# Optimization experiments

Measured on AMD Instinct MI355X. Metric: run time of the kernel, lower is better.

## Reference

```python
import math
import jax, jax.numpy as jnp
import numpy as np

B, N, D = 16, 2048, 256
EPS = 1e-8  # torch cosine_similarity default eps
TAU = 3.0   # gumbel-softmax temperature


def setup_inputs() -> dict:
    key = jax.random.key(0)
    k1, k2 = jax.random.split(key)
    return {
        "LowLevelFeatures": jax.random.normal(k1, (B, 1, N, D), dtype=jnp.float32),
        "HighLevelFeatures": jax.random.normal(k2, (B, 1, N, D), dtype=jnp.float32),
        "batch_size": B,
    }


def _forward(LLF4, HLF4):
    LLF = LLF4[:, 0]  # [B,N,D]
    HLF = HLF4[:, 0]  # [B,N,D]
    b, n, d = LLF.shape
    # pairwise cosine similarity [B,N,N]: matmul + norm-product (same math as
    # torch's broadcast cosine_similarity, without the [B,N,N,D] intermediate)
    dots = jnp.einsum('bnd,bmd->bnm', LLF, HLF)
    nl = jnp.linalg.norm(LLF, axis=-1)  # [B,N]
    nh = jnp.linalg.norm(HLF, axis=-1)  # [B,N]
    sim = dots / jnp.maximum(nl[:, :, None] * nh[:, None, :], EPS)
    sim = sim / math.sqrt(d)
    probs = jax.nn.softmax(sim, axis=1)  # softmax over dim 1 (LLF rows)
    # F.gumbel_softmax(probs, tau=3, hard=True, dim=1): probs act as logits
    u = jax.random.uniform(jax.random.key(42), probs.shape,
                           minval=1e-10, maxval=1.0)
    gumbels = -jnp.log(-jnp.log(u))
    y_soft = jax.nn.softmax((probs + gumbels) / TAU, axis=1)
    idx = jnp.argmax(y_soft, axis=1)  # [B,N]: selected LLF-row n per HLF col m
    # torch.where on the one-hot scans row-major over (b, n, m), so per batch
    # the returned n-indices are the SORTED multiset of selected indices
    sl = jnp.sort(idx, axis=-1)  # [B,N]
    bidx = jnp.arange(b)[:, None]  # [B,1]
    aligned = HLF[bidx, sl]  # gather along dim 1 -> [B,N,D]
    # rowwise cosine similarity between gathered HLF and LLF
    w = jnp.sum(aligned * LLF, axis=-1) / jnp.maximum(
        jnp.linalg.norm(aligned, axis=-1) * nl, EPS)  # [B,N]
    noise = jax.nn.softmax(w / 0.1, axis=1)[:, :, None]  # [B,N,1]
    hlf_new = aligned + LLF * noise
    out = HLF.at[bidx, sl].set(hlf_new)
    return out


def reference(LowLevelFeatures, HighLevelFeatures, batch_size):
    return _forward(LowLevelFeatures, HighLevelFeatures)
```

## Files before the change

### kernel.cpp

```cpp
#include <hip/hip_runtime.h>
#include <math.h>

#define NB 16
#define NN 2048
#define ND 256
#define BNtot (NB*NN)
#define HH 33554432u

__device__ __forceinline__ unsigned rotl(unsigned v, int r){
  return __builtin_amdgcn_alignbit(v, v, 32-r);
}
__device__ __forceinline__ unsigned umaxu(unsigned a, unsigned b){ return a > b ? a : b; }
__device__ __forceinline__ unsigned uminu(unsigned a, unsigned b){ return a < b ? a : b; }

__device__ __forceinline__ float gumbelv(unsigned b, unsigned n, unsigned m){
  unsigned f = (b<<22) | (n<<11) | m;
  unsigned x0 = (b < 8u) ? f : (f - HH);
  unsigned x1 = x0 + HH;
  const unsigned ks0=0u, ks1=42u, ks2=0u^42u^0x1BD11BDAu;
  unsigned v0 = x0 + ks0;
  unsigned v1 = x1 + ks1;
#define TFR(r) { v0 += v1; v1 = rotl(v1,(r)); v1 ^= v0; }
  TFR(13) TFR(15) TFR(26) TFR(6)
  v0 += ks1; v1 += ks2 + 1u;
  TFR(17) TFR(29) TFR(16) TFR(24)
  v0 += ks2; v1 += ks0 + 2u;
  TFR(13) TFR(15) TFR(26) TFR(6)
  v0 += ks0; v1 += ks1 + 3u;
  TFR(17) TFR(29) TFR(16) TFR(24)
  v0 += ks1; v1 += ks2 + 4u;
  TFR(13) TFR(15) TFR(26) TFR(6)
  v0 += ks2; v1 += ks0 + 5u;
#undef TFR
  unsigned bits = (b < 8u) ? v0 : v1;
  float fl = __uint_as_float((bits>>9) | 0x3F800000u) - 1.0f;
  float u = fmaxf(1e-10f, fl + 1e-10f);
  return -logf(-logf(u));
}

__device__ __forceinline__ float gfromkey(unsigned key){
  float fl = __uint_as_float(key | 0x3F800000u) - 1.0f;
  float u = fmaxf(1e-10f, fl + 1e-10f);
  return -logf(-logf(u));
}

struct GumState {
  unsigned x0, vk, a1, a2, c1, c2;
  int t;
};

__device__ __forceinline__ void gum_init(GumState& g, int t){
  g.t = t;
  int half = t & 1;
  int m    = (t >> 1) & 2047;
  int bl   = (t >> 12) & 7;
  int nq   = t >> 15;
  int nstart = (nq << 7) + (half << 6);
  g.x0 = ((unsigned)bl << 22) | ((unsigned)nstart << 11) | (unsigned)m;
  g.a1 = g.a2 = g.c1 = g.c2 = 0;
  g.vk = (unsigned)(127 - (half<<6));
}

__device__ __forceinline__ void gum_iter(GumState& g, const int cnt){
  const unsigned KS2 = 42u ^ 0x1BD11BDAu;
  unsigned x0=g.x0, vk=g.vk, a1=g.a1, a2=g.a2, c1=g.c1, c2=g.c2;
#define TFR(r)       { v0 += v1; v1 = rotl(v1,(r)); v1 ^= v0; }
#define TFRI(r, inj) { v0 += v1 + (inj); v1 = rotl(v1,(r)); v1 ^= v0; }
  #pragma unroll 4
  for (int j = 0; j < cnt; ++j){
    unsigned v0 = x0;
    unsigned v1 = x0 + (HH + 42u);
    TFR(13) TFR(15) TFR(26) TFR(6)
    v1 += KS2 + 1u;
    TFRI(17, 42u) TFR(29) TFR(16) TFR(24)
    v1 += 2u;
    TFRI(13, KS2) TFR(15) TFR(26) TFR(6)
    v1 += 42u + 3u;
    TFR(17) TFR(29) TFR(16) TFR(24)
    v1 += KS2 + 4u;
    TFRI(13, 42u) TFR(15) TFR(26) TFR(6)
    v0 += KS2; v1 += 5u;
    unsigned pa = (v0 & 0xFFFFFE00u) | vk;
    unsigned pb = (v1 & 0xFFFFFE00u) | vk;
    unsigned ta = uminu(pa, a1);
    a1 = umaxu(pa, a1);
    a2 = umaxu(ta, a2);
    unsigned tc = uminu(pb, c1);
    c1 = umaxu(pb, c1);
    c2 = umaxu(tc, c2);
    x0 += 2048u;
    vk -= 1u;
  }
#undef TFR
#undef TFRI
  g.x0=x0; g.vk=vk; g.a1=a1; g.a2=a2; g.c1=c1; g.c2=c2;
}

__device__ __forceinline__ void gum_finish(const GumState& g, unsigned* __restrict__ pck){
  int half = g.t & 1;
  int m    = (g.t >> 1) & 2047;
  int bl   = (g.t >> 12) & 7;
  int nq   = g.t >> 15;
  unsigned p1 = __shfl_xor((int)g.a1, 1), p2 = __shfl_xor((int)g.a2, 1);
  unsigned q1 = __shfl_xor((int)g.c1, 1), q2 = __shfl_xor((int)g.c2, 1);
  unsigned A1 = umaxu(g.a1, p1);
  unsigned A2 = umaxu(uminu(g.a1, p1), umaxu(g.a2, p2));
  unsigned C1 = umaxu(g.c1, q1);
  unsigned C2 = umaxu(uminu(g.c1, q1), umaxu(g.c2, q2));
  if (half == 0){
    uint2 ua; ua.x = A1; ua.y = A2;
    uint2 uc; uc.x = C1; uc.y = C2;
    *(uint2*)(&pck[((size_t)bl*NN + m)*32 + (nq<<1)])     = ua;
    *(uint2*)(&pck[((size_t)(bl+8)*NN + m)*32 + (nq<<1)]) = uc;
  }
}

__device__ __forceinline__ void norm_rows(const float4* v, int wid, int lane,
                                          float* __restrict__ nrm){
  #pragma unroll
  for (int i=0;i<4;i++){
    float s = v[i].x*v[i].x + v[i].y*v[i].y + v[i].z*v[i].z + v[i].w*v[i].w;
    for (int o=32;o;o>>=1) s += __shfl_down(s,o);
    if (lane==0) nrm[wid*4 + i] = sqrtf(s);
  }
}

__global__ void knorms(const float* __restrict__ LLF, const float* __restrict__ HLF,
                       float* __restrict__ nl, float* __restrict__ nh){
  int row = blockIdx.x;
  int wave = threadIdx.x >> 6;
  int lane = threadIdx.x & 63;
  const float* src = wave ? HLF : LLF;
  float4 v = ((const float4*)(src + (size_t)row*ND))[lane];
  float s = v.x*v.x + v.y*v.y + v.z*v.z + v.w*v.w;
  for (int o=32;o;o>>=1) s += __shfl_down(s,o);
  if (lane==0) (wave? nh: nl)[row] = sqrtf(s);
}

__launch_bounds__(256, 8)
__global__ void kfuse1(const float* __restrict__ LLF, const float* __restrict__ HLF,
                       float* __restrict__ nl, float* __restrict__ nh,
                       unsigned* __restrict__ pck){
  int t = blockIdx.x*256 + (int)threadIdx.x;
  int wid = t >> 6;
  int lane = t & 63;
  GumState g; gum_init(g, t);
  float4 va[4];
  #pragma unroll
  for (int i=0;i<4;i++)
    va[i] = ((const float4*)(LLF + (size_t)(wid*4+i)*ND))[lane];
  gum_iter(g, 32);
  norm_rows(va, wid, lane, nl);
  float4 vb[4];
  #pragma unroll
  for (int i=0;i<4;i++)
    vb[i] = ((const float4*)(HLF + (size_t)(wid*4+i)*ND))[lane];
  gum_iter(g, 32);
  norm_rows(vb, wid, lane, nh);
  gum_finish(g, pck);
}

#define ILO 4.882e-4f
#define IHI 5.534e-4f
__launch_bounds__(256)
__global__ void kresolve(const float* __restrict__ LLF, const float* __restrict__ HLF,
                         const float* __restrict__ nl, const float* __restrict__ nh,
                         const unsigned* __restrict__ pck,
                         int* __restrict__ idx){
  __shared__ float hsAll[4][ND];
  int w    = threadIdx.x >> 6;
  int lane = threadIdx.x & 63;
  int g = blockIdx.x*4 + w;
  int b = g >> 11;
  float pv = -INFINITY; int pn = 0;
  if (lane < 32){
    unsigned pk = pck[(size_t)g*32 + lane];
    pv = gfromkey(pk >> 9);
    pn = ((lane >> 1) << 7) + 127 - (int)(pk & 127u);
  }
  float gmax = pv;
  for (int o=32;o;o>>=1) gmax = fmaxf(gmax, __shfl_down(gmax,o));
  gmax = __shfl(gmax, 0);
  unsigned long long mask = __ballot(pv >= gmax - 8e-5f) & 0xFFFFFFFFull;
  if (__popcll(mask) == 1){
    int src = __builtin_ctzll(mask);
    int n = __shfl(pn, src);
    if (lane==0) idx[g] = n;
    return;
  }
  float4 h = ((const float4*)(HLF + (size_t)g*ND))[lane];
  float nhg = nh[g];
  float bestLo = -INFINITY, bestHi = -INFINITY;
  int nLo = 1<<30, nHi = 1<<30;
  unsigned long long mm = mask;
  while (mm){
    int src = __builtin_ctzll(mm); mm &= mm-1;
    int   n  = __shfl(pn, src);
    float gv = __shfl(pv, src);
    float4 a = ((const float4*)(LLF + ((size_t)b*NN + n)*ND))[lane];
    float d = a.x*h.x + a.y*h.y + a.z*h.z + a.w*h.w;
    for (int o=32;o;o>>=1) d += __shfl_down(d,o);
    d = __shfl(d, 0);
    float sim = (d / fmaxf(nl[b*NN+n]*nhg, 1e-8f)) * 0.0625f;
    float e = expf(sim - 0.0625f);
    float qlo = e*ILO + gv;
    float qhi = e*IHI + gv;
    if (qlo > bestLo || (qlo == bestLo && n < nLo)){ bestLo = qlo; nLo = n; }
    if (qhi > bestHi || (qhi == bestHi && n < nHi)){ bestHi = qhi; nHi = n; }
  }
  if (nLo == nHi){
    if (lane==0) idx[g] = nLo;
    return;
  }
  float* hs = hsAll[w];
  *(float4*)(&hs[lane<<2]) = h;
  float S = 0.0f;
  for (int r = 0; r < 32; ++r){
    int n2 = (r<<6) + lane;
    const float4* ap = (const float4*)(LLF + ((size_t)b*NN + n2)*ND);
    float dd0=0.f, dd1=0.f, dd2=0.f, dd3=0.f;
    #pragma unroll 4
    for (int k=0;k<64;k+=4){
      float4 a0=ap[k], a1=ap[k+1], a2=ap[k+2], a3=ap[k+3];
      dd0 += a0.x*hs[4*k+ 0]+a0.y*hs[4*k+ 1]+a0.z*hs[4*k+ 2]+a0.w*hs[4*k+ 3];
      dd1 += a1.x*hs[4*k+ 4]+a1.y*hs[4*k+ 5]+a1.z*hs[4*k+ 6]+a1.w*hs[4*k+ 7];
      dd2 += a2.x*hs[4*k+ 8]+a2.y*hs[4*k+ 9]+a2.z*hs[4*k+10]+a2.w*hs[4*k+11];
      dd3 += a3.x*hs[4*k+12]+a3.y*hs[4*k+13]+a3.z*hs[4*k+14]+a3.w*hs[4*k+15];
    }
    float d = (dd0+dd1)+(dd2+dd3);
    float sim = (d / fmaxf(nl[b*NN+n2]*nhg, 1e-8f)) * 0.0625f;
    S += expf(sim - 0.0625f);
  }
  for (int o=32;o;o>>=1) S += __shfl_down(S,o);
  S = __shfl(S, 0);
  float invS = 1.0f / S;
  float bestQ = -INFINITY; int bestN = 1<<30;
  mm = mask;
  while (mm){
    int src = __builtin_ctzll(mm); mm &= mm-1;
    int   n  = __shfl(pn, src);
    float gv = __shfl(pv, src);
    float4 a = ((const float4*)(LLF + ((size_t)b*NN + n)*ND))[lane];
    float d = a.x*h.x + a.y*h.y + a.z*h.z + a.w*h.w;
    for (int o=32;o;o>>=1) d += __shfl_down(d,o);
    d = __shfl(d, 0);
    float sim = (d / fmaxf(nl[b*NN+n]*nhg, 1e-8f)) * 0.0625f;
    float q = expf(sim - 0.0625f)*invS + gv;
    if (q > bestQ || (q == bestQ && n < bestN)){ bestQ = q; bestN = n; }
  }
  if (lane==0) idx[g] = bestN;
}

__launch_bounds__(256)
__global__ void kstats(const float* __restrict__ A, const float* __restrict__ Bm,
                       const float* __restrict__ nl, const float* __restrict__ nh,
                       float* __restrict__ Mout, float* __restrict__ Sinv){
  __shared__ float As[64][33];
  __shared__ float Bs[64][33];
  __shared__ float Cs[64][65];
  const int b  = blockIdx.x >> 5;
  const int m0 = (blockIdx.x & 31) << 6;
  const float* Ab = A  + (size_t)b*NN*ND;
  const float* Bb = Bm + (size_t)b*NN*ND;
  const int tid = threadIdx.x;
  const int tx = tid & 15, ty = tid >> 4;
  float nhv[4];
  #pragma unroll
  for (int j=0;j<4;j++) nhv[j] = nh[b*NN + m0 + tx*4 + j];
  float Mr = -INFINITY, Sr = 0.0f;
  for (int nt=0; nt<NN; nt+=64){
    float acc[4][4] = {{0.f,0.f,0.f,0.f},{0.f,0.f,0.f,0.f},{0.f,0.f,0.f,0.f},{0.f,0.f,0.f,0.f}};
    for (int kc=0; kc<ND; kc+=32){
      __syncthreads();
      #pragma unroll
      for (int s=0;s<2;s++){
        int f = tid + (s<<8);
        int r = f >> 3;
        int c = (f & 7) << 2;
        float4 va = *(const float4*)(Ab + (size_t)(nt+r)*ND + kc + c);
        As[r][c]=va.x; As[r][c+1]=va.y; As[r][c+2]=va.z; As[r][c+3]=va.w;
        float4 vb = *(const float4*)(Bb + (size_t)(m0+r)*ND + kc + c);
        Bs[r][c]=vb.x; Bs[r][c+1]=vb.y; Bs[r][c+2]=vb.z; Bs[r][c+3]=vb.w;
      }
      __syncthreads();
      #pragma unroll 4
      for (int k=0;k<32;k++){
        float a0=As[ty*4+0][k], a1=As[ty*4+1][k], a2=As[ty*4+2][k], a3=As[ty*4+3][k];
        float b0=Bs[tx*4+0][k], b1=Bs[tx*4+1][k], b2=Bs[tx*4+2][k], b3=Bs[tx*4+3][k];
        acc[0][0]+=a0*b0; acc[0][1]+=a0*b1; acc[0][2]+=a0*b2; acc[0][3]+=a0*b3;
        acc[1][0]+=a1*b0; acc[1][1]+=a1*b1; acc[1][2]+=a1*b2; acc[1][3]+=a1*b3;
        acc[2][0]+=a2*b0; acc[2][1]+=a2*b1; acc[2][2]+=a2*b2; acc[2][3]+=a2*b3;
        acc[3][0]+=a3*b0; acc[3][1]+=a3*b1; acc[3][2]+=a3*b2; acc[3][3]+=a3*b3;
      }
    }
    float nlv[4];
    #pragma unroll
    for (int i=0;i<4;i++) nlv[i] = nl[b*NN + nt + ty*4 + i];
    __syncthreads();
    #pragma unroll
    for (int i=0;i<4;i++)
      #pragma unroll
      for (int j=0;j<4;j++){
        float denom = fmaxf(nlv[i]*nhv[j], 1e-8f);
        Cs[ty*4+i][tx*4+j] = (acc[i][j]/denom)*0.0625f;
      }
    __syncthreads();
    if (tid < 64){
      float tmax = -INFINITY;
      #pragma unroll 8
      for (int r=0;r<64;r++) tmax = fmaxf(tmax, Cs[r][tid]);
      float newM = fmaxf(Mr, tmax);
      float s = 0.0f;
      #pragma unroll 4
      for (int r=0;r<64;r++) s += expf(Cs[r][tid]-newM);
      Sr = Sr*expf(Mr-newM) + s;
      Mr = newM;
    }
  }
  if (tid < 64){
    Mout[b*NN+m0+tid] = Mr;
    Sinv[b*NN+m0+tid] = 1.0f/Sr;
  }
}

__launch_bounds__(256)
__global__ void kargmax(const float* __restrict__ A, const float* __restrict__ Bm,
                        const float* __restrict__ nl, const float* __restrict__ nh,
                        const float* __restrict__ Mv, const float* __restrict__ Sv,
                        int* __restrict__ idxout){
  __shared__ float As[64][33];
  __shared__ float Bs[64][33];
  __shared__ float Vs[16][64];
  __shared__ int   Is[16][64];
  const int b  = blockIdx.x >> 5;
  const int m0 = (blockIdx.x & 31) << 6;
  const float* Ab = A  + (size_t)b*NN*ND;
  const float* Bb = Bm + (size_t)b*NN*ND;
  const int tid = threadIdx.x;
  const int tx = tid & 15, ty = tid >> 4;
  float nhv[4], Mj[4], iSj[4];
  #pragma unroll
  for (int j=0;j<4;j++){
    int m = m0 + tx*4 + j;
    nhv[j] = nh[b*NN + m];
    Mj[j]  = Mv[b*NN + m];
    iSj[j] = Sv[b*NN + m];
  }
  float bestV = -INFINITY; int bestN = 0;
  for (int nt=0; nt<NN; nt+=64){
    float acc[4][4] = {{0.f,0.f,0.f,0.f},{0.f,0.f,0.f,0.f},{0.f,0.f,0.f,0.f},{0.f,0.f,0.f,0.f}};
    for (int kc=0; kc<ND; kc+=32){
      __syncthreads();
      #pragma unroll
      for (int s=0;s<2;s++){
        int f = tid + (s<<8);
        int r = f >> 3;
        int c = (f & 7) << 2;
        float4 va = *(const float4*)(Ab + (size_t)(nt+r)*ND + kc + c);
        As[r][c]=va.x; As[r][c+1]=va.y; As[r][c+2]=va.z; As[r][c+3]=va.w;
        float4 vb = *(const float4*)(Bb + (size_t)(m0+r)*ND + kc + c);
        Bs[r][c]=vb.x; Bs[r][c+1]=vb.y; Bs[r][c+2]=vb.z; Bs[r][c+3]=vb.w;
      }
      __syncthreads();
      #pragma unroll 4
      for (int k=0;k<32;k++){
        float a0=As[ty*4+0][k], a1=As[ty*4+1][k], a2=As[ty*4+2][k], a3=As[ty*4+3][k];
        float b0=Bs[tx*4+0][k], b1=Bs[tx*4+1][k], b2=Bs[tx*4+2][k], b3=Bs[tx*4+3][k];
        acc[0][0]+=a0*b0; acc[0][1]+=a0*b1; acc[0][2]+=a0*b2; acc[0][3]+=a0*b3;
        acc[1][0]+=a1*b0; acc[1][1]+=a1*b1; acc[1][2]+=a1*b2; acc[1][3]+=a1*b3;
        acc[2][0]+=a2*b0; acc[2][1]+=a2*b1; acc[2][2]+=a2*b2; acc[2][3]+=a2*b3;
        acc[3][0]+=a3*b0; acc[3][1]+=a3*b1; acc[3][2]+=a3*b2; acc[3][3]+=a3*b3;
      }
    }
    float nlv[4];
    #pragma unroll
    for (int i=0;i<4;i++) nlv[i] = nl[b*NN + nt + ty*4 + i];
    float lv[4]; int li[4];
    #pragma unroll
    for (int j=0;j<4;j++){ lv[j] = -INFINITY; li[j] = 0; }
    #pragma unroll
    for (int i=0;i<4;i++){
      int n = nt + ty*4 + i;
      #pragma unroll
      for (int j=0;j<4;j++){
        float denom = fmaxf(nlv[i]*nhv[j], 1e-8f);
        float sim = (acc[i][j]/denom)*0.0625f;
        float p = expf(sim - Mj[j]) * iSj[j];
        float v = p + gumbelv((unsigned)b, (unsigned)n, (unsigned)(m0 + tx*4 + j));
        if (v > lv[j]) { lv[j] = v; li[j] = n; }
      }
    }
    __syncthreads();
    #pragma unroll
    for (int j=0;j<4;j++){ Vs[ty][tx*4+j]=lv[j]; Is[ty][tx*4+j]=li[j]; }
    __syncthreads();
    if (tid < 64){
      #pragma unroll 4
      for (int t=0;t<16;t++){
        float v = Vs[t][tid];
        if (v > bestV){ bestV = v; bestN = Is[t][tid]; }
      }
    }
  }
  if (tid < 64) idxout[b*NN + m0 + tid] = bestN;
}

__global__ void ksort(const int* __restrict__ idx, int* __restrict__ cntg,
                      int* __restrict__ offg, int* __restrict__ sl){
  __shared__ int c[NN];
  __shared__ int part[256];
  int b = blockIdx.x, tid = threadIdx.x;
  for (int v=tid; v<NN; v+=256) c[v]=0;
  __syncthreads();
  for (int j=tid; j<NN; j+=256) atomicAdd(&c[idx[b*NN+j]], 1);
  __syncthreads();
  int base = tid*8, s=0, lc[8];
  #pragma unroll
  for (int k=0;k<8;k++){ lc[k]=c[base+k]; s+=lc[k]; }
  part[tid]=s; __syncthreads();
  for (int o=1;o<256;o<<=1){
    int v = (tid>=o)? part[tid-o] : 0;
    __syncthreads();
    part[tid]+=v;
    __syncthreads();
  }
  int run = part[tid]-s;
  #pragma unroll
  for (int k=0;k<8;k++){
    int v = base+k;
    cntg[b*NN+v]=lc[k];
    offg[b*NN+v]=run;
    for (int j=0;j<lc[k];j++) sl[b*NN+run+j]=v;
    run += lc[k];
  }
}

__global__ void kw(const float* __restrict__ LLF, const float* __restrict__ HLF,
                   const float* __restrict__ nl, const float* __restrict__ nh,
                   const int* __restrict__ sl, float* __restrict__ w){
  int g = blockIdx.x*4 + (threadIdx.x>>6);
  int lane = threadIdx.x & 63;
  int b = g >> 11;
  int s = sl[g];
  float4 a = ((const float4*)(HLF + ((size_t)b*NN + s)*ND))[lane];
  float4 l = ((const float4*)(LLF + (size_t)g*ND))[lane];
  float d = a.x*l.x + a.y*l.y + a.z*l.z + a.w*l.w;
  for (int o=32;o;o>>=1) d += __shfl_down(d,o);
  if (lane==0){
    float denom = fmaxf(nh[b*NN+s]*nl[g], 1e-8f);
    w[g] = d/denom;
  }
}

__global__ void knoise(const float* __restrict__ w, float* __restrict__ nz){
  int b = blockIdx.x, tid = threadIdx.x;
  __shared__ float sred[4];
  float x[8]; float mx = -INFINITY;
  #pragma unroll
  for (int k=0;k<8;k++){ x[k] = w[b*NN + tid*8 + k] / 0.1f; mx = fmaxf(mx, x[k]); }
  for (int o=32;o;o>>=1) mx = fmaxf(mx, __shfl_down(mx,o));
  mx = __shfl(mx, 0);
  if ((tid&63)==0) sred[tid>>6] = mx;
  __syncthreads();
  mx = fmaxf(fmaxf(sred[0],sred[1]), fmaxf(sred[2],sred[3]));
  __syncthreads();
  float e[8]; float s = 0.f;
  #pragma unroll
  for (int k=0;k<8;k++){ e[k] = expf(x[k]-mx); s += e[k]; }
  for (int o=32;o;o>>=1) s += __shfl_down(s,o);
  s = __shfl(s, 0);
  if ((tid&63)==0) sred[tid>>6] = s;
  __syncthreads();
  s = sred[0]+sred[1]+sred[2]+sred[3];
  #pragma unroll
  for (int k=0;k<8;k++) nz[b*NN + tid*8 + k] = e[k]/s;
}

__global__ void kfinal(const float* __restrict__ LLF, const float* __restrict__ HLF,
                       const int* __restrict__ cnt, const int* __restrict__ off,
                       const float* __restrict__ nz, float* __restrict__ out){
  int row = blockIdx.x;
  int lane = threadIdx.x;
  int b = row >> 11;
  float4 h = ((const float4*)(HLF + (size_t)row*ND))[lane];
  int c = cnt[row];
  if (c > 0){
    int i = off[row] + c - 1;
    float ns = nz[b*NN + i];
    float4 l = ((const float4*)(LLF + ((size_t)(b*NN + i))*ND))[lane];
    h.x += l.x*ns; h.y += l.y*ns; h.z += l.z*ns; h.w += l.w*ns;
  }
  ((float4*)(out + (size_t)row*ND))[lane] = h;
}

extern "C" void kernel_launch(void* const* d_in, const int* in_sizes, int n_in,
                              void* d_out, int out_size, void* d_ws, size_t ws_size,
                              hipStream_t stream){
  const float* LLF = (const float*)d_in[0];
  const float* HLF = (const float*)d_in[1];
  float* out = (float*)d_out;
  float* ws = (float*)d_ws;

  float* nl  = ws;
  float* nh  = ws + 1*(size_t)BNtot;
  float* iS  = ws + 2*(size_t)BNtot;
  int*   idx = (int*)(ws + 3*(size_t)BNtot);
  int*   cnt = (int*)(ws + 4*(size_t)BNtot);
  int*   off = (int*)(ws + 5*(size_t)BNtot);
  int*   sl  = (int*)(ws + 6*(size_t)BNtot);
  float* wv  = ws + 7*(size_t)BNtot;
  float* nz  = ws + 8*(size_t)BNtot;
  unsigned* pck = (unsigned*)(ws + 9*(size_t)BNtot);
  const size_t needA = (9 + 32) * (size_t)BNtot * 4;

  if (ws_size >= needA){
    hipLaunchKernelGGL(kfuse1,  dim3(2048),    dim3(256), 0, stream, LLF, HLF, nl, nh, pck);
    hipLaunchKernelGGL(kresolve,dim3(BNtot/4), dim3(256), 0, stream, LLF, HLF, nl, nh, pck, idx);
  } else {
    float* Mv = ws + 9*(size_t)BNtot;
    hipLaunchKernelGGL(knorms,   dim3(BNtot),    dim3(128), 0, stream, LLF, HLF, nl, nh);
    hipLaunchKernelGGL(kstats,   dim3(NB*32),    dim3(256), 0, stream, LLF, HLF, nl, nh, Mv, iS);
    hipLaunchKernelGGL(kargmax,  dim3(NB*32),    dim3(256), 0, stream, LLF, HLF, nl, nh, Mv, iS, idx);
  }

  hipLaunchKernelGGL(ksort,  dim3(NB),      dim3(256), 0, stream, idx, cnt, off, sl);
  hipLaunchKernelGGL(kw,     dim3(BNtot/4), dim3(256), 0, stream, LLF, HLF, nl, nh, sl, wv);
  hipLaunchKernelGGL(knoise, dim3(NB),      dim3(256), 0, stream, wv, nz);
  hipLaunchKernelGGL(kfinal, dim3(BNtot),   dim3(64),  0, stream, LLF, HLF, cnt, off, nz, out);
}
```

Baseline: 333.8 us.

## Share full-column softmax sum across all four waves of the resolve block

In the resolve kernel, rows that still need the exact softmax denominator are now recorded in shared memory. The whole 256-thread block then computes each such row's 2048-entry sum cooperatively, instead of the single owning wave doing all 32 iterations alone. This is meant to cut the tail latency when a few waves in a block hit the slow path while the others finish early. In exchange it adds block-wide barriers and serialises the pending rows across the block, so it pays off only if slow-path rows are rare.

```diff
diff --git a/kernel.cpp b/kernel.cpp
--- a/kernel.cpp
+++ b/kernel.cpp
@@ -168,6 +168,8 @@
                          const unsigned* __restrict__ pck,
                          int* __restrict__ idx){
   __shared__ float hsAll[4][ND];
+  __shared__ int   needLDS[4];
+  __shared__ float Sres[4];
   int w    = threadIdx.x >> 6;
   int lane = threadIdx.x & 63;
   int g = blockIdx.x*4 + w;
@@ -182,73 +184,91 @@
   for (int o=32;o;o>>=1) gmax = fmaxf(gmax, __shfl_down(gmax,o));
   gmax = __shfl(gmax, 0);
   unsigned long long mask = __ballot(pv >= gmax - 8e-5f) & 0xFFFFFFFFull;
+  int resolved = -1;
+  int need = -1;
+  float4 h = {0.f,0.f,0.f,0.f};
+  float nhg = 1.0f;
   if (__popcll(mask) == 1){
     int src = __builtin_ctzll(mask);
-    int n = __shfl(pn, src);
-    if (lane==0) idx[g] = n;
-    return;
-  }
-  float4 h = ((const float4*)(HLF + (size_t)g*ND))[lane];
-  float nhg = nh[g];
-  float bestLo = -INFINITY, bestHi = -INFINITY;
-  int nLo = 1<<30, nHi = 1<<30;
-  unsigned long long mm = mask;
-  while (mm){
-    int src = __builtin_ctzll(mm); mm &= mm-1;
-    int   n  = __shfl(pn, src);
-    float gv = __shfl(pv, src);
-    float4 a = ((const float4*)(LLF + ((size_t)b*NN + n)*ND))[lane];
-    float d = a.x*h.x + a.y*h.y + a.z*h.z + a.w*h.w;
-    for (int o=32;o;o>>=1) d += __shfl_down(d,o);
-    d = __shfl(d, 0);
-    float sim = (d / fmaxf(nl[b*NN+n]*nhg, 1e-8f)) * 0.0625f;
-    float e = expf(sim - 0.0625f);
-    float qlo = e*ILO + gv;
-    float qhi = e*IHI + gv;
-    if (qlo > bestLo || (qlo == bestLo && n < nLo)){ bestLo = qlo; nLo = n; }
-    if (qhi > bestHi || (qhi == bestHi && n < nHi)){ bestHi = qhi; nHi = n; }
-  }
-  if (nLo == nHi){
-    if (lane==0) idx[g] = nLo;
-    return;
-  }
-  float* hs = hsAll[w];
-  *(float4*)(&hs[lane<<2]) = h;
-  float S = 0.0f;
-  for (int r = 0; r < 32; ++r){
-    int n2 = (r<<6) + lane;
-    const float4* ap = (const float4*)(LLF + ((size_t)b*NN + n2)*ND);
-    float dd0=0.f, dd1=0.f, dd2=0.f, dd3=0.f;
-    #pragma unroll 4
-    for (int k=0;k<64;k+=4){
-      float4 a0=ap[k], a1=ap[k+1], a2=ap[k+2], a3=ap[k+3];
-      dd0 += a0.x*hs[4*k+ 0]+a0.y*hs[4*k+ 1]+a0.z*hs[4*k+ 2]+a0.w*hs[4*k+ 3];
-      dd1 += a1.x*hs[4*k+ 4]+a1.y*hs[4*k+ 5]+a1.z*hs[4*k+ 6]+a1.w*hs[4*k+ 7];
-      dd2 += a2.x*hs[4*k+ 8]+a2.y*hs[4*k+ 9]+a2.z*hs[4*k+10]+a2.w*hs[4*k+11];
-      dd3 += a3.x*hs[4*k+12]+a3.y*hs[4*k+13]+a3.z*hs[4*k+14]+a3.w*hs[4*k+15];
-    }
-    float d = (dd0+dd1)+(dd2+dd3);
-    float sim = (d / fmaxf(nl[b*NN+n2]*nhg, 1e-8f)) * 0.0625f;
-    S += expf(sim - 0.0625f);
-  }
-  for (int o=32;o;o>>=1) S += __shfl_down(S,o);
-  S = __shfl(S, 0);
-  float invS = 1.0f / S;
-  float bestQ = -INFINITY; int bestN = 1<<30;
-  mm = mask;
-  while (mm){
-    int src = __builtin_ctzll(mm); mm &= mm-1;
-    int   n  = __shfl(pn, src);
-    float gv = __shfl(pv, src);
-    float4 a = ((const float4*)(LLF + ((size_t)b*NN + n)*ND))[lane];
-    float d = a.x*h.x + a.y*h.y + a.z*h.z + a.w*h.w;
-    for (int o=32;o;o>>=1) d += __shfl_down(d,o);
-    d = __shfl(d, 0);
-    float sim = (d / fmaxf(nl[b*NN+n]*nhg, 1e-8f)) * 0.0625f;
-    float q = expf(sim - 0.0625f)*invS + gv;
-    if (q > bestQ || (q == bestQ && n < bestN)){ bestQ = q; bestN = n; }
-  }
-  if (lane==0) idx[g] = bestN;
+    resolved = __shfl(pn, src);
+  } else {
+    h = ((const float4*)(HLF + (size_t)g*ND))[lane];
+    *(float4*)(&hsAll[w][lane<<2]) = h;
+    nhg = nh[g];
+    float bestLo = -INFINITY, bestHi = -INFINITY;
+    int nLo = 1<<30, nHi = 1<<30;
+    unsigned long long mm = mask;
+    while (mm){
+      int src = __builtin_ctzll(mm); mm &= mm-1;
+      int   n  = __shfl(pn, src);
+      float gv = __shfl(pv, src);
+      float4 a = ((const float4*)(LLF + ((size_t)b*NN + n)*ND))[lane];
+      float d = a.x*h.x + a.y*h.y + a.z*h.z + a.w*h.w;
+      for (int o=32;o;o>>=1) d += __shfl_down(d,o);
+      d = __shfl(d, 0);
+      float sim = (d / fmaxf(nl[b*NN+n]*nhg, 1e-8f)) * 0.0625f;
+      float e = expf(sim - 0.0625f);
+      float qlo = e*ILO + gv;
+      float qhi = e*IHI + gv;
+      if (qlo > bestLo || (qlo == bestLo && n < nLo)){ bestLo = qlo; nLo = n; }
+      if (qhi > bestHi || (qhi == bestHi && n < nHi)){ bestHi = qhi; nHi = n; }
+    }
+    if (nLo == nHi) resolved = nLo; else need = g;
+  }
+  if (resolved >= 0 && lane == 0) idx[g] = resolved;
+  if (lane == 0) needLDS[w] = need;
+  __syncthreads();
+  int nm = needLDS[0] > needLDS[1] ? needLDS[0] : needLDS[1];
+  int nm2 = needLDS[2] > needLDS[3] ? needLDS[2] : needLDS[3];
+  if ((nm > nm2 ? nm : nm2) < 0) return;
+
+  for (int w2 = 0; w2 < 4; ++w2){
+    int g2 = needLDS[w2];
+    if (g2 < 0) continue;
+    int b2 = g2 >> 11;
+    float nh2 = nh[g2];
+    const float* hs = hsAll[w2];
+    float S = 0.0f;
+    for (int r = 0; r < 8; ++r){
+      int n2 = (r<<8) + (int)threadIdx.x;
+      const float4* ap = (const float4*)(LLF + ((size_t)b2*NN + n2)*ND);
+      float dd0=0.f, dd1=0.f, dd2=0.f, dd3=0.f;
+      #pragma unroll 4
+      for (int k=0;k<64;k+=4){
+        float4 a0=ap[k], a1=ap[k+1], a2=ap[k+2], a3=ap[k+3];
+        dd0 += a0.x*hs[4*k+ 0]+a0.y*hs[4*k+ 1]+a0.z*hs[4*k+ 2]+a0.w*hs[4*k+ 3];
+        dd1 += a1.x*hs[4*k+ 4]+a1.y*hs[4*k+ 5]+a1.z*hs[4*k+ 6]+a1.w*hs[4*k+ 7];
+        dd2 += a2.x*hs[4*k+ 8]+a2.y*hs[4*k+ 9]+a2.z*hs[4*k+10]+a2.w*hs[4*k+11];
+        dd3 += a3.x*hs[4*k+12]+a3.y*hs[4*k+13]+a3.z*hs[4*k+14]+a3.w*hs[4*k+15];
+      }
+      float d = (dd0+dd1)+(dd2+dd3);
+      float sim = (d / fmaxf(nl[b2*NN+n2]*nh2, 1e-8f)) * 0.0625f;
+      S += expf(sim - 0.0625f);
+    }
+    for (int o=32;o;o>>=1) S += __shfl_down(S,o);
+    if (lane == 0) Sres[w] = S;
+    __syncthreads();
+    float Stot = (Sres[0]+Sres[1])+(Sres[2]+Sres[3]);
+    if (w == w2){
+      float invS = 1.0f / Stot;
+      float bestQ = -INFINITY; int bestN = 1<<30;
+      unsigned long long mm = mask;
+      while (mm){
+        int src = __builtin_ctzll(mm); mm &= mm-1;
+        int   n  = __shfl(pn, src);
+        float gv = __shfl(pv, src);
+        float4 a = ((const float4*)(LLF + ((size_t)b*NN + n)*ND))[lane];
+        float d = a.x*h.x + a.y*h.y + a.z*h.z + a.w*h.w;
+        for (int o=32;o;o>>=1) d += __shfl_down(d,o);
+        d = __shfl(d, 0);
+        float sim = (d / fmaxf(nl[b*NN+n]*nhg, 1e-8f)) * 0.0625f;
+        float q = expf(sim - 0.0625f)*invS + gv;
+        if (q > bestQ || (q == bestQ && n < bestN)){ bestQ = q; bestN = n; }
+      }
+      if (lane == 0) idx[g] = bestN;
+    }
+    __syncthreads();
+  }
 }
 
 __launch_bounds__(256)
```

Measured after the change: 276.7 us. -17.1%, faster.
